# Optimization experiments

Hardware: AMD Instinct MI355X
Metric: run time of the kernel (lower is better)

The kernel has to match this reference:

```python
import jax, jax.numpy as jnp
import numpy as np

NUM_TREES = 150
ARITY = 4
DEPTH = 4
NUM_LEVELS = DEPTH + 1  # leaves (level 0) ... root (level DEPTH)
VOCAB = 10000
SUBTOK = 8
EMB_DIM = 256
HID = 256
NUM_CLASSES = 2


def _build_forest():
    # perfect ARITY-ary tree, level-order indexing; edges point child -> parent
    n = (ARITY ** (DEPTH + 1) - 1) // (ARITY - 1)  # 341
    src = np.arange(1, n)
    dst = (src - 1) // ARITY
    depth_of = np.zeros(n, dtype=np.int64)
    for j in range(1, n):
        depth_of[j] = depth_of[(j - 1) // ARITY] + 1
    level_of = DEPTH - depth_of  # leaves = 0, processed first (topo order)
    offs = np.arange(NUM_TREES) * n
    edge_src = (src[None, :] + offs[:, None]).ravel().astype(np.int32)
    edge_dst = (dst[None, :] + offs[:, None]).ravel().astype(np.int32)
    node_level = np.tile(level_of, NUM_TREES).astype(np.int32)
    graph_id = np.repeat(np.arange(NUM_TREES), n).astype(np.int32)
    leaf_mask = (node_level == 0).astype(np.int32)
    return edge_src, edge_dst, node_level, graph_id, leaf_mask, NUM_TREES * n


def setup_inputs() -> dict:
    key = jax.random.key(0)
    ks = jax.random.split(key, 16)
    es, ed, lvl, gid, lm, N = _build_forest()
    s_e = 1.0 / np.sqrt(EMB_DIM)
    s_h = 1.0 / np.sqrt(HID)
    s_f = 1.0 / np.sqrt(2 * HID)
    return {
        "node_feat1": jax.random.randint(ks[0], (N, SUBTOK), 0, VOCAB, dtype=jnp.int32),
        "node_feat2": jax.random.randint(ks[1], (N, SUBTOK), 0, VOCAB, dtype=jnp.int32),
        "emb1": jax.random.normal(ks[2], (VOCAB, EMB_DIM), jnp.float32) * 0.02,
        "emb2": jax.random.normal(ks[3], (VOCAB, EMB_DIM), jnp.float32) * 0.02,
        "W_iou1": jax.random.normal(ks[4], (EMB_DIM, 3 * HID), jnp.float32) * s_e,
        "W_iou2": jax.random.normal(ks[5], (EMB_DIM, 3 * HID), jnp.float32) * s_e,
        "U_iou1": jax.random.normal(ks[6], (HID, 3 * HID), jnp.float32) * s_h,
        "U_iou2": jax.random.normal(ks[7], (HID, 3 * HID), jnp.float32) * s_h,
        "Uf_W1": jax.random.normal(ks[8], (HID, HID), jnp.float32) * s_h,
        "Uf_b1": jnp.zeros((HID,), jnp.float32),
        "Uf_W2": jax.random.normal(ks[9], (HID, HID), jnp.float32) * s_h,
        "Uf_b2": jnp.zeros((HID,), jnp.float32),
        "b_iou1": jnp.zeros((3 * HID,), jnp.float32),
        "b_iou2": jnp.zeros((3 * HID,), jnp.float32),
        "Wf": jax.random.normal(ks[10], (2 * HID, NUM_CLASSES), jnp.float32) * s_f,
        "bf": jnp.zeros((NUM_CLASSES,), jnp.float32),
        "edge_src": jnp.asarray(es),
        "edge_dst": jnp.asarray(ed),
        "node_level": jnp.asarray(lvl),
        "graph_id": jnp.asarray(gid),
        "leaf_mask": jnp.asarray(lm),
    }


def _tree_lstm(iou0, U_iou, Uf_W, Uf_b, b_iou, edge_src, edge_dst, node_level):
    # ChildSum TreeLSTM, propagated level-by-level (leaves -> root)
    N = iou0.shape[0]
    h = jnp.zeros((N, HID), iou0.dtype)
    c = jnp.zeros((N, HID), iou0.dtype)
    for lvl in range(NUM_LEVELS):
        emask = (node_level[edge_dst] == lvl).astype(h.dtype)[:, None]  # [E,1]
        hs = h[edge_src] * emask  # children h (already computed at lower levels)
        f = jax.nn.sigmoid(hs @ Uf_W + Uf_b)  # per-edge forget gate
        h_tild = jax.ops.segment_sum(hs, edge_dst, num_segments=N)
        c_sum = jax.ops.segment_sum(f * c[edge_src] * emask, edge_dst, num_segments=N)
        has_child = jax.ops.segment_sum(emask, edge_dst, num_segments=N) > 0  # [N,1]
        # DGL semantics: reduce overwrites iou for internal nodes; leaves keep W_iou(x)*mask
        iou = jnp.where(has_child, h_tild @ U_iou, iou0) + b_iou
        i, o, u = jnp.split(iou, 3, axis=1)
        c_new = jax.nn.sigmoid(i) * jnp.tanh(u) + c_sum
        h_new = jax.nn.sigmoid(o) * jnp.tanh(c_new)
        at = (node_level == lvl)[:, None]
        h = jnp.where(at, h_new, h)
        c = jnp.where(at, c_new, c)
    return h


def _branch(node_feat, emb, W_iou, U_iou, Uf_W, Uf_b, b_iou,
            leaf_mask, edge_src, edge_dst, node_level, graph_id):
    embeds = emb[node_feat].mean(axis=1)  # subtoken mean pooling -> [N, EMB_DIM]
    iou0 = (embeds @ W_iou) * leaf_mask.astype(embeds.dtype)[:, None]
    h = _tree_lstm(iou0, U_iou, Uf_W, Uf_b, b_iou, edge_src, edge_dst, node_level)
    s = jax.ops.segment_sum(h, graph_id, num_segments=NUM_TREES)
    cnt = jax.ops.segment_sum(jnp.ones((h.shape[0],), h.dtype), graph_id, num_segments=NUM_TREES)
    return jax.nn.relu(s / cnt[:, None])  # mean graph readout + relu


def reference(node_feat1, node_feat2, emb1, emb2, W_iou1, W_iou2, U_iou1, U_iou2,
              Uf_W1, Uf_b1, Uf_W2, Uf_b2, b_iou1, b_iou2, Wf, bf,
              edge_src, edge_dst, node_level, graph_id, leaf_mask):
    m1 = _branch(node_feat1, emb1, W_iou1, U_iou1, Uf_W1, Uf_b1, b_iou1,
                 leaf_mask, edge_src, edge_dst, node_level, graph_id)
    m2 = _branch(node_feat2, emb2, W_iou2, U_iou2, Uf_W2, Uf_b2, b_iou2,
                 leaf_mask, edge_src, edge_dst, node_level, graph_id)
    logits = jax.nn.leaky_relu(jnp.concatenate([m1, m2], axis=1) @ Wf + bf, 0.01)
    return jax.nn.softmax(logits, axis=-1)
```

## Files before the change

### kernel.cpp

```cpp
#include <hip/hip_runtime.h>

#define NT 150
#define NPT 341
#define LEAF0 85
#define NL (NT*256)
#define NN (NT*NPT)
#define VOCAB 10000

typedef __attribute__((ext_vector_type(8))) short short8;
typedef __attribute__((ext_vector_type(4))) float floatx4;

__device__ __forceinline__ float sigf(float x){ return 1.0f/(1.0f+__expf(-x)); }
__device__ __forceinline__ float bf2f(ushort u){ union{unsigned i; float f;} v; v.i = ((unsigned)u)<<16; return v.f; }
__device__ __forceinline__ ushort f2bf(float x){ union{float f; unsigned i;} v; v.f = x; return (ushort)((v.i + 0x7fff + ((v.i>>16)&1))>>16); }

__global__ __launch_bounds__(256) void convW_k(
    const float* __restrict__ W1, const float* __restrict__ U1, const float* __restrict__ F1,
    const float* __restrict__ W2, const float* __restrict__ U2, const float* __restrict__ F2,
    ushort* Wt1, ushort* Ut1, ushort* Ft1, ushort* Wt2, ushort* Ut2, ushort* Ft2){
  __shared__ float T[32][33];
  const float* src; ushort* dst; int N;
  switch (blockIdx.z){
    case 0: src=W1; dst=Wt1; N=768; break;
    case 1: src=U1; dst=Ut1; N=768; break;
    case 2: src=F1; dst=Ft1; N=256; break;
    case 3: src=W2; dst=Wt2; N=768; break;
    case 4: src=U2; dst=Ut2; N=768; break;
    default: src=F2; dst=Ft2; N=256; break;
  }
  int n0 = blockIdx.x*32; if (n0 >= N) return;
  int k0 = blockIdx.y*32;
  int nl = threadIdx.x & 31, kb = threadIdx.x >> 5;
  #pragma unroll
  for (int i=0;i<4;i++){ int kk = kb*4+i; T[kk][nl] = src[(size_t)(k0+kk)*N + n0 + nl]; }
  __syncthreads();
  #pragma unroll
  for (int i=0;i<4;i++){ int nn = kb*4+i; dst[(size_t)(n0+nn)*256 + k0 + nl] = f2bf(T[nl][nn]); }
}

__global__ __launch_bounds__(256) void convE_k(
    const float* __restrict__ e1, const float* __restrict__ e2,
    ushort* __restrict__ E1, ushort* __restrict__ E2){
  const float* s = blockIdx.y ? e2 : e1;
  ushort* d = blockIdx.y ? E2 : E1;
  size_t i = ((size_t)blockIdx.x*256 + threadIdx.x)*4;
  float4 v = *(const float4*)&s[i];
  d[i+0]=f2bf(v.x); d[i+1]=f2bf(v.y); d[i+2]=f2bf(v.z); d[i+3]=f2bf(v.w);
}

__global__ __launch_bounds__(256) void embed_k(
    const int* __restrict__ f1, const int* __restrict__ f2,
    const ushort* __restrict__ E1, const ushort* __restrict__ E2,
    ushort* __restrict__ h1, ushort* __restrict__ h2){
  int br = blockIdx.y;
  const int* feat = br ? f2 : f1;
  const ushort* E = br ? E2 : E1;
  ushort* h = br ? h2 : h1;
  int t = threadIdx.x;
  int leaf = blockIdx.x*16 + (t>>4);
  int seg = t & 15;
  int tree = leaf >> 8;
  size_t node = (size_t)tree*NPT + LEAF0 + (leaf & 255);
  const int* f = feat + node*8;
  float s[16];
  #pragma unroll
  for (int q=0;q<16;q++) s[q]=0.f;
  #pragma unroll
  for (int j=0;j<8;j++){
    const ushort* row = E + (size_t)f[j]*256 + seg*16;
    short8 a = *(const short8*)row;
    short8 b = *(const short8*)(row+8);
    #pragma unroll
    for (int q=0;q<8;q++){ s[q]+=bf2f((ushort)a[q]); s[8+q]+=bf2f((ushort)b[q]); }
  }
  short8 o1, o2;
  #pragma unroll
  for (int q=0;q<8;q++){ o1[q]=(short)f2bf(s[q]*0.125f); o2[q]=(short)f2bf(s[8+q]*0.125f); }
  ushort* dst = h + node*256 + seg*16;
  *(short8*)dst = o1; *(short8*)(dst+8) = o2;
}

__global__ __launch_bounds__(1024) void leaf_gemm(
    const ushort* __restrict__ Wt1, const float* __restrict__ b1,
    const ushort* __restrict__ Wt2, const float* __restrict__ b2,
    ushort* __restrict__ h1, ushort* __restrict__ c1,
    ushort* __restrict__ h2, ushort* __restrict__ c2){
  __shared__ __attribute__((aligned(16))) ushort As[8][64*40];
  int br = blockIdx.y;
  const ushort* Wt = br ? Wt2 : Wt1;
  const float* biou = br ? b2 : b1;
  ushort* h = br ? h2 : h1;
  ushort* c = br ? c2 : c1;
  int tid = threadIdx.x;
  int lane = tid & 63, wav = tid >> 6, quad = lane >> 4, l15 = lane & 15;
  int rowbase = blockIdx.x*64;

  {
    int row = tid >> 4, seg = tid & 15;
    int leaf = rowbase + row;
    int tree = leaf >> 8;
    size_t node = (size_t)tree*NPT + LEAF0 + (leaf & 255);
    const ushort* src = h + node*256 + seg*16;
    short8 a = *(const short8*)src;
    short8 b = *(const short8*)(src+8);
    int cch = seg >> 1, off = (seg & 1)*16;
    *(short8*)&As[cch][row*40 + off]     = a;
    *(short8*)&As[cch][row*40 + off + 8] = b;
  }
  __syncthreads();

  floatx4 acc[3][4];
  #pragma unroll
  for (int g=0;g<3;g++)
    #pragma unroll
    for (int r=0;r<4;r++) acc[g][r] = (floatx4){0.f,0.f,0.f,0.f};

  const ushort* bp0 = Wt + (size_t)(0*256 + wav*16 + l15)*256 + quad*8;
  const ushort* bp1 = Wt + (size_t)(1*256 + wav*16 + l15)*256 + quad*8;
  const ushort* bp2 = Wt + (size_t)(2*256 + wav*16 + l15)*256 + quad*8;

  #pragma unroll
  for (int cch=0; cch<8; cch++){
    short8 b0 = *(const short8*)(bp0 + cch*32);
    short8 b1 = *(const short8*)(bp1 + cch*32);
    short8 b2 = *(const short8*)(bp2 + cch*32);
    #pragma unroll
    for (int r=0;r<4;r++){
      short8 a = *(const short8*)&As[cch][(16*r + l15)*40 + quad*8];
      acc[0][r] = __builtin_amdgcn_mfma_f32_16x16x32_bf16(a, b0, acc[0][r], 0,0,0);
      acc[1][r] = __builtin_amdgcn_mfma_f32_16x16x32_bf16(a, b1, acc[1][r], 0,0,0);
      acc[2][r] = __builtin_amdgcn_mfma_f32_16x16x32_bf16(a, b2, acc[2][r], 0,0,0);
    }
  }
  int hc = wav*16 + l15;
  float bi = biou[hc], bo = biou[256+hc], bu = biou[512+hc];
  #pragma unroll
  for (int r=0;r<4;r++){
    #pragma unroll
    for (int reg=0;reg<4;reg++){
      int leaf = rowbase + 16*r + quad*4 + reg;
      int tree = leaf >> 8;
      size_t node = (size_t)tree*NPT + LEAF0 + (leaf & 255);
      float iv = acc[0][r][reg] + bi;
      float ov = acc[1][r][reg] + bo;
      float uv = acc[2][r][reg] + bu;
      float cc = sigf(iv)*tanhf(uv);
      float hh = sigf(ov)*tanhf(cc);
      h[node*256 + hc] = f2bf(hh);
      c[node*256 + hc] = f2bf(cc);
    }
  }
}

__global__ __launch_bounds__(256) void level_k(
    const ushort* __restrict__ Ut1, const ushort* __restrict__ Ft1,
    const float* __restrict__ Ufb1, const float* __restrict__ bi1,
    const ushort* __restrict__ Ut2, const ushort* __restrict__ Ft2,
    const float* __restrict__ Ufb2, const float* __restrict__ bi2,
    ushort* __restrict__ h1, ushort* __restrict__ c1,
    ushort* __restrict__ h2, ushort* __restrict__ c2,
    int M, int shift, int base){
  __shared__ __attribute__((aligned(16))) ushort Ch[8][64*40];
  int br = blockIdx.z;
  const ushort* Ut = br ? Ut2 : Ut1;
  const ushort* Ft = br ? Ft2 : Ft1;
  const float* Ufb = br ? Ufb2 : Ufb1;
  const float* biou = br ? bi2 : bi1;
  ushort* h = br ? h2 : h1;
  ushort* c = br ? c2 : c1;
  int tid = threadIdx.x;
  int lane = tid & 63, wav = tid >> 6, quad = lane >> 4, l15 = lane & 15;
  int m0 = blockIdx.x*16, cb = blockIdx.y;
  int mask = (1<<shift)-1;

  {
    int cl = tid >> 2, q4 = tid & 3;
    int sm = m0 + (cl >> 2); if (sm > M-1) sm = M-1;
    int stree = sm >> shift, sloc = base + (sm & mask);
    const ushort* sgp = h + ((size_t)stree*NPT + 4*sloc + 1 + (cl & 3))*256 + q4*8;
    #pragma unroll
    for (int cc=0;cc<8;cc++)
      *(short8*)&Ch[cc][cl*40 + q4*8] = *(const short8*)(sgp + cc*32);
  }
  __syncthreads();

  int col = cb*64 + wav*16 + l15;
  const ushort* bfp = Ft + (size_t)col*256 + quad*8;
  const ushort* bp0 = Ut + (size_t)(0*256 + col)*256 + quad*8;
  const ushort* bp1 = Ut + (size_t)(256 + col)*256 + quad*8;
  const ushort* bp2 = Ut + (size_t)(512 + col)*256 + quad*8;

  floatx4 af[4], ai[4], ao[4], au[4];
  #pragma unroll
  for (int r=0;r<4;r++){
    af[r] = (floatx4){0.f,0.f,0.f,0.f}; ai[r] = (floatx4){0.f,0.f,0.f,0.f};
    ao[r] = (floatx4){0.f,0.f,0.f,0.f}; au[r] = (floatx4){0.f,0.f,0.f,0.f};
  }

  #pragma unroll
  for (int cc=0; cc<8; cc++){
    short8 Bf = *(const short8*)(bfp + cc*32);
    short8 Bi = *(const short8*)(bp0 + cc*32);
    short8 Bo = *(const short8*)(bp1 + cc*32);
    short8 Bu = *(const short8*)(bp2 + cc*32);
    #pragma unroll
    for (int r=0;r<4;r++){
      short8 a = *(const short8*)&Ch[cc][(16*r + l15)*40 + quad*8];
      af[r] = __builtin_amdgcn_mfma_f32_16x16x32_bf16(a, Bf, af[r], 0,0,0);
      ai[r] = __builtin_amdgcn_mfma_f32_16x16x32_bf16(a, Bi, ai[r], 0,0,0);
      ao[r] = __builtin_amdgcn_mfma_f32_16x16x32_bf16(a, Bo, ao[r], 0,0,0);
      au[r] = __builtin_amdgcn_mfma_f32_16x16x32_bf16(a, Bu, au[r], 0,0,0);
    }
  }

  float ufb = Ufb[col];
  float bI = biou[col], bO = biou[256+col], bU = biou[512+col];
  #pragma unroll
  for (int r=0;r<4;r++){
    int m = m0 + 4*r + quad;
    int mm = m < M ? m : M-1;
    int tree = mm >> shift, loc = base + (mm & mask);
    size_t ch0 = ((size_t)tree*NPT + 4*loc + 1)*256 + col;
    float cs = 0.f;
    #pragma unroll
    for (int reg=0;reg<4;reg++)
      cs += sigf(af[r][reg] + ufb) * bf2f(c[ch0 + (size_t)reg*256]);
    float iv = ai[r][0]+ai[r][1]+ai[r][2]+ai[r][3] + bI;
    float ov = ao[r][0]+ao[r][1]+ao[r][2]+ao[r][3] + bO;
    float uv = au[r][0]+au[r][1]+au[r][2]+au[r][3] + bU;
    float cn = sigf(iv)*tanhf(uv) + cs;
    float hn = sigf(ov)*tanhf(cn);
    if (m < M){
      size_t off = ((size_t)tree*NPT + loc)*256 + col;
      h[off] = f2bf(hn);
      c[off] = f2bf(cn);
    }
  }
}

__global__ __launch_bounds__(256) void readout_k(
    const ushort* __restrict__ h1, const ushort* __restrict__ h2,
    float* __restrict__ mp1, float* __restrict__ mp2){
  int br = blockIdx.z, part = blockIdx.y, tree = blockIdx.x;
  const ushort* h = br ? h2 : h1;
  float* mp = br ? mp2 : mp1;
  int t = threadIdx.x;
  int start = part*85;
  int cnt = (part==3) ? 86 : 85;
  const ushort* hp = h + ((size_t)tree*NPT + start)*256 + t;
  float s0=0.f,s1=0.f,s2=0.f,s3=0.f;
  int i = 0;
  for (; i+4<=cnt; i+=4){
    s0 += bf2f(hp[(size_t)(i+0)*256]); s1 += bf2f(hp[(size_t)(i+1)*256]);
    s2 += bf2f(hp[(size_t)(i+2)*256]); s3 += bf2f(hp[(size_t)(i+3)*256]);
  }
  for (; i<cnt; i++) s0 += bf2f(hp[(size_t)i*256]);
  mp[((size_t)tree*4 + part)*256 + t] = s0+s1+s2+s3;
}

__global__ __launch_bounds__(64) void final_k(const float* __restrict__ mp1,
    const float* __restrict__ mp2, const float* __restrict__ Wf,
    const float* __restrict__ bf, float* __restrict__ out){
  int tree = blockIdx.x; int t = threadIdx.x;
  float p0=0.f, p1=0.f;
  for (int k=t;k<512;k+=64){
    const float* mp = (k<256) ? mp1 : mp2;
    int kk = k & 255;
    size_t b0 = ((size_t)tree*4)*256 + kk;
    float s = mp[b0] + mp[b0+256] + mp[b0+512] + mp[b0+768];
    float x = fmaxf(s*(1.0f/341.0f), 0.f);
    p0 += x*Wf[k*2+0]; p1 += x*Wf[k*2+1];
  }
  #pragma unroll
  for (int off=32; off>0; off>>=1){
    p0 += __shfl_down(p0, off);
    p1 += __shfl_down(p1, off);
  }
  if (t==0){
    float l0 = p0+bf[0], l1 = p1+bf[1];
    l0 = (l0>0.f)?l0:0.01f*l0;
    l1 = (l1>0.f)?l1:0.01f*l1;
    float mx = fmaxf(l0,l1);
    float e0 = __expf(l0-mx), e1 = __expf(l1-mx);
    float inv = 1.0f/(e0+e1);
    out[tree*2+0] = e0*inv; out[tree*2+1] = e1*inv;
  }
}

extern "C" void kernel_launch(void* const* d_in, const int* in_sizes, int n_in,
                              void* d_out, int out_size, void* d_ws, size_t ws_size,
                              hipStream_t stream) {
  const int*   feat1 = (const int*)  d_in[0];
  const int*   feat2 = (const int*)  d_in[1];
  const float* emb1  = (const float*)d_in[2];
  const float* emb2  = (const float*)d_in[3];
  const float* Wiou1 = (const float*)d_in[4];
  const float* Wiou2 = (const float*)d_in[5];
  const float* Uiou1 = (const float*)d_in[6];
  const float* Uiou2 = (const float*)d_in[7];
  const float* UfW1  = (const float*)d_in[8];
  const float* Ufb1  = (const float*)d_in[9];
  const float* UfW2  = (const float*)d_in[10];
  const float* Ufb2  = (const float*)d_in[11];
  const float* biou1 = (const float*)d_in[12];
  const float* biou2 = (const float*)d_in[13];
  const float* Wf    = (const float*)d_in[14];
  const float* bfv   = (const float*)d_in[15];
  float* out = (float*)d_out;

  char* ws = (char*)d_ws;
  ushort* h1  = (ushort*)ws;  ws += (size_t)NN*256*2;
  ushort* h2  = (ushort*)ws;  ws += (size_t)NN*256*2;
  ushort* c1  = (ushort*)ws;  ws += (size_t)NN*256*2;
  ushort* c2  = (ushort*)ws;  ws += (size_t)NN*256*2;
  ushort* E1  = (ushort*)ws;  ws += (size_t)VOCAB*256*2;
  ushort* E2  = (ushort*)ws;  ws += (size_t)VOCAB*256*2;
  ushort* Wt1 = (ushort*)ws;  ws += 768*256*2;
  ushort* Ut1 = (ushort*)ws;  ws += 768*256*2;
  ushort* Ft1 = (ushort*)ws;  ws += 256*256*2;
  ushort* Wt2 = (ushort*)ws;  ws += 768*256*2;
  ushort* Ut2 = (ushort*)ws;  ws += 768*256*2;
  ushort* Ft2 = (ushort*)ws;  ws += 256*256*2;
  float*  mp1 = (float*)ws;   ws += (size_t)NT*4*256*4;
  float*  mp2 = (float*)ws;   ws += (size_t)NT*4*256*4;

  convW_k<<<dim3(24, 8, 6), 256, 0, stream>>>(Wiou1, Uiou1, UfW1, Wiou2, Uiou2, UfW2,
                                              Wt1, Ut1, Ft1, Wt2, Ut2, Ft2);
  convE_k<<<dim3(2500, 2), 256, 0, stream>>>(emb1, emb2, E1, E2);
  embed_k<<<dim3(NL/16, 2), 256, 0, stream>>>(feat1, feat2, E1, E2, h1, h2);
  leaf_gemm<<<dim3(NL/64, 2), 1024, 0, stream>>>(Wt1, biou1, Wt2, biou2, h1, c1, h2, c2);

  const int lvlM[4]     = {9600, 2400, 600, 150};
  const int lvlShift[4] = {6, 4, 2, 0};
  const int lvlBase[4]  = {21, 5, 1, 0};
  for (int l=0;l<4;l++){
    int gx = (lvlM[l] + 15)/16;
    level_k<<<dim3(gx, 4, 2), 256, 0, stream>>>(Ut1, Ft1, Ufb1, biou1,
                                                Ut2, Ft2, Ufb2, biou2,
                                                h1, c1, h2, c2,
                                                lvlM[l], lvlShift[l], lvlBase[l]);
  }
  readout_k<<<dim3(NT, 4, 2), 256, 0, stream>>>(h1, h2, mp1, mp2);
  final_k<<<NT, 64, 0, stream>>>(mp1, mp2, Wf, bfv, out);
}
```

Measured before the change: 380.8 us.

## Fuse embedding pooling into leaf GEMM and reuse child tiles across column blocks

```diff
diff --git a/kernel.cpp b/kernel.cpp
--- a/kernel.cpp
+++ b/kernel.cpp
@@ -48,45 +48,17 @@
   d[i+0]=f2bf(v.x); d[i+1]=f2bf(v.y); d[i+2]=f2bf(v.z); d[i+3]=f2bf(v.w);
 }
 
-__global__ __launch_bounds__(256) void embed_k(
+__global__ __launch_bounds__(1024) void leaf_k(
     const int* __restrict__ f1, const int* __restrict__ f2,
     const ushort* __restrict__ E1, const ushort* __restrict__ E2,
-    ushort* __restrict__ h1, ushort* __restrict__ h2){
-  int br = blockIdx.y;
-  const int* feat = br ? f2 : f1;
-  const ushort* E = br ? E2 : E1;
-  ushort* h = br ? h2 : h1;
-  int t = threadIdx.x;
-  int leaf = blockIdx.x*16 + (t>>4);
-  int seg = t & 15;
-  int tree = leaf >> 8;
-  size_t node = (size_t)tree*NPT + LEAF0 + (leaf & 255);
-  const int* f = feat + node*8;
-  float s[16];
-  #pragma unroll
-  for (int q=0;q<16;q++) s[q]=0.f;
-  #pragma unroll
-  for (int j=0;j<8;j++){
-    const ushort* row = E + (size_t)f[j]*256 + seg*16;
-    short8 a = *(const short8*)row;
-    short8 b = *(const short8*)(row+8);
-    #pragma unroll
-    for (int q=0;q<8;q++){ s[q]+=bf2f((ushort)a[q]); s[8+q]+=bf2f((ushort)b[q]); }
-  }
-  short8 o1, o2;
-  #pragma unroll
-  for (int q=0;q<8;q++){ o1[q]=(short)f2bf(s[q]*0.125f); o2[q]=(short)f2bf(s[8+q]*0.125f); }
-  ushort* dst = h + node*256 + seg*16;
-  *(short8*)dst = o1; *(short8*)(dst+8) = o2;
-}
-
-__global__ __launch_bounds__(1024) void leaf_gemm(
     const ushort* __restrict__ Wt1, const float* __restrict__ b1,
     const ushort* __restrict__ Wt2, const float* __restrict__ b2,
     ushort* __restrict__ h1, ushort* __restrict__ c1,
     ushort* __restrict__ h2, ushort* __restrict__ c2){
   __shared__ __attribute__((aligned(16))) ushort As[8][64*40];
   int br = blockIdx.y;
+  const int* feat = br ? f2 : f1;
+  const ushort* E = br ? E2 : E1;
   const ushort* Wt = br ? Wt2 : Wt1;
   const float* biou = br ? b2 : b1;
   ushort* h = br ? h2 : h1;
@@ -100,12 +72,24 @@
     int leaf = rowbase + row;
     int tree = leaf >> 8;
     size_t node = (size_t)tree*NPT + LEAF0 + (leaf & 255);
-    const ushort* src = h + node*256 + seg*16;
-    short8 a = *(const short8*)src;
-    short8 b = *(const short8*)(src+8);
+    const int* f = feat + node*8;
+    float s[16];
+    #pragma unroll
+    for (int q=0;q<16;q++) s[q]=0.f;
+    #pragma unroll
+    for (int j=0;j<8;j++){
+      const ushort* rp = E + (size_t)f[j]*256 + seg*16;
+      short8 a = *(const short8*)rp;
+      short8 b = *(const short8*)(rp+8);
+      #pragma unroll
+      for (int q=0;q<8;q++){ s[q]+=bf2f((ushort)a[q]); s[8+q]+=bf2f((ushort)b[q]); }
+    }
+    short8 o1, o2;
+    #pragma unroll
+    for (int q=0;q<8;q++){ o1[q]=(short)f2bf(s[q]*0.125f); o2[q]=(short)f2bf(s[8+q]*0.125f); }
     int cch = seg >> 1, off = (seg & 1)*16;
-    *(short8*)&As[cch][row*40 + off]     = a;
-    *(short8*)&As[cch][row*40 + off + 8] = b;
+    *(short8*)&As[cch][row*40 + off]     = o1;
+    *(short8*)&As[cch][row*40 + off + 8] = o2;
   }
   __syncthreads();
 
@@ -159,7 +143,7 @@
     const float* __restrict__ Ufb2, const float* __restrict__ bi2,
     ushort* __restrict__ h1, ushort* __restrict__ c1,
     ushort* __restrict__ h2, ushort* __restrict__ c2,
-    int M, int shift, int base){
+    int M, int shift, int base, int ncb){
   __shared__ __attribute__((aligned(16))) ushort Ch[8][64*40];
   int br = blockIdx.z;
   const ushort* Ut = br ? Ut2 : Ut1;
@@ -170,7 +154,8 @@
   ushort* c = br ? c2 : c1;
   int tid = threadIdx.x;
   int lane = tid & 63, wav = tid >> 6, quad = lane >> 4, l15 = lane & 15;
-  int m0 = blockIdx.x*16, cb = blockIdx.y;
+  int m0 = blockIdx.x*16;
+  int cb0 = blockIdx.y*ncb;
   int mask = (1<<shift)-1;
 
   {
@@ -184,56 +169,58 @@
   }
   __syncthreads();
 
-  int col = cb*64 + wav*16 + l15;
-  const ushort* bfp = Ft + (size_t)col*256 + quad*8;
-  const ushort* bp0 = Ut + (size_t)(0*256 + col)*256 + quad*8;
-  const ushort* bp1 = Ut + (size_t)(256 + col)*256 + quad*8;
-  const ushort* bp2 = Ut + (size_t)(512 + col)*256 + quad*8;
-
-  floatx4 af[4], ai[4], ao[4], au[4];
-  #pragma unroll
-  for (int r=0;r<4;r++){
-    af[r] = (floatx4){0.f,0.f,0.f,0.f}; ai[r] = (floatx4){0.f,0.f,0.f,0.f};
-    ao[r] = (floatx4){0.f,0.f,0.f,0.f}; au[r] = (floatx4){0.f,0.f,0.f,0.f};
-  }
-
-  #pragma unroll
-  for (int cc=0; cc<8; cc++){
-    short8 Bf = *(const short8*)(bfp + cc*32);
-    short8 Bi = *(const short8*)(bp0 + cc*32);
-    short8 Bo = *(const short8*)(bp1 + cc*32);
-    short8 Bu = *(const short8*)(bp2 + cc*32);
+  for (int p=0; p<ncb; p++){
+    int col = (cb0+p)*64 + wav*16 + l15;
+    const ushort* bfp = Ft + (size_t)col*256 + quad*8;
+    const ushort* bp0 = Ut + (size_t)(0*256 + col)*256 + quad*8;
+    const ushort* bp1 = Ut + (size_t)(256 + col)*256 + quad*8;
+    const ushort* bp2 = Ut + (size_t)(512 + col)*256 + quad*8;
+
+    floatx4 af[4], ai[4], ao[4], au[4];
     #pragma unroll
     for (int r=0;r<4;r++){
-      short8 a = *(const short8*)&Ch[cc][(16*r + l15)*40 + quad*8];
-      af[r] = __builtin_amdgcn_mfma_f32_16x16x32_bf16(a, Bf, af[r], 0,0,0);
-      ai[r] = __builtin_amdgcn_mfma_f32_16x16x32_bf16(a, Bi, ai[r], 0,0,0);
-      ao[r] = __builtin_amdgcn_mfma_f32_16x16x32_bf16(a, Bo, ao[r], 0,0,0);
-      au[r] = __builtin_amdgcn_mfma_f32_16x16x32_bf16(a, Bu, au[r], 0,0,0);
-    }
-  }
-
-  float ufb = Ufb[col];
-  float bI = biou[col], bO = biou[256+col], bU = biou[512+col];
-  #pragma unroll
-  for (int r=0;r<4;r++){
-    int m = m0 + 4*r + quad;
-    int mm = m < M ? m : M-1;
-    int tree = mm >> shift, loc = base + (mm & mask);
-    size_t ch0 = ((size_t)tree*NPT + 4*loc + 1)*256 + col;
-    float cs = 0.f;
-    #pragma unroll
-    for (int reg=0;reg<4;reg++)
-      cs += sigf(af[r][reg] + ufb) * bf2f(c[ch0 + (size_t)reg*256]);
-    float iv = ai[r][0]+ai[r][1]+ai[r][2]+ai[r][3] + bI;
-    float ov = ao[r][0]+ao[r][1]+ao[r][2]+ao[r][3] + bO;
-    float uv = au[r][0]+au[r][1]+au[r][2]+au[r][3] + bU;
-    float cn = sigf(iv)*tanhf(uv) + cs;
-    float hn = sigf(ov)*tanhf(cn);
-    if (m < M){
-      size_t off = ((size_t)tree*NPT + loc)*256 + col;
-      h[off] = f2bf(hn);
-      c[off] = f2bf(cn);
+      af[r] = (floatx4){0.f,0.f,0.f,0.f}; ai[r] = (floatx4){0.f,0.f,0.f,0.f};
+      ao[r] = (floatx4){0.f,0.f,0.f,0.f}; au[r] = (floatx4){0.f,0.f,0.f,0.f};
+    }
+
+    #pragma unroll
+    for (int cc=0; cc<8; cc++){
+      short8 Bf = *(const short8*)(bfp + cc*32);
+      short8 Bi = *(const short8*)(bp0 + cc*32);
+      short8 Bo = *(const short8*)(bp1 + cc*32);
+      short8 Bu = *(const short8*)(bp2 + cc*32);
+      #pragma unroll
+      for (int r=0;r<4;r++){
+        short8 a = *(const short8*)&Ch[cc][(16*r + l15)*40 + quad*8];
+        af[r] = __builtin_amdgcn_mfma_f32_16x16x32_bf16(a, Bf, af[r], 0,0,0);
+        ai[r] = __builtin_amdgcn_mfma_f32_16x16x32_bf16(a, Bi, ai[r], 0,0,0);
+        ao[r] = __builtin_amdgcn_mfma_f32_16x16x32_bf16(a, Bo, ao[r], 0,0,0);
+        au[r] = __builtin_amdgcn_mfma_f32_16x16x32_bf16(a, Bu, au[r], 0,0,0);
+      }
+    }
+
+    float ufb = Ufb[col];
+    float bI = biou[col], bO = biou[256+col], bU = biou[512+col];
+    #pragma unroll
+    for (int r=0;r<4;r++){
+      int m = m0 + 4*r + quad;
+      int mm = m < M ? m : M-1;
+      int tree = mm >> shift, loc = base + (mm & mask);
+      size_t ch0 = ((size_t)tree*NPT + 4*loc + 1)*256 + col;
+      float cs = 0.f;
+      #pragma unroll
+      for (int reg=0;reg<4;reg++)
+        cs += sigf(af[r][reg] + ufb) * bf2f(c[ch0 + (size_t)reg*256]);
+      float iv = ai[r][0]+ai[r][1]+ai[r][2]+ai[r][3] + bI;
+      float ov = ao[r][0]+ao[r][1]+ao[r][2]+ao[r][3] + bO;
+      float uv = au[r][0]+au[r][1]+au[r][2]+au[r][3] + bU;
+      float cn = sigf(iv)*tanhf(uv) + cs;
+      float hn = sigf(ov)*tanhf(cn);
+      if (m < M){
+        size_t off = ((size_t)tree*NPT + loc)*256 + col;
+        h[off] = f2bf(hn);
+        c[off] = f2bf(cn);
+      }
     }
   }
 }
@@ -324,21 +311,23 @@
   float*  mp1 = (float*)ws;   ws += (size_t)NT*4*256*4;
   float*  mp2 = (float*)ws;   ws += (size_t)NT*4*256*4;
 
+  convE_k<<<dim3(2500, 2), 256, 0, stream>>>(emb1, emb2, E1, E2);
   convW_k<<<dim3(24, 8, 6), 256, 0, stream>>>(Wiou1, Uiou1, UfW1, Wiou2, Uiou2, UfW2,
                                               Wt1, Ut1, Ft1, Wt2, Ut2, Ft2);
-  convE_k<<<dim3(2500, 2), 256, 0, stream>>>(emb1, emb2, E1, E2);
-  embed_k<<<dim3(NL/16, 2), 256, 0, stream>>>(feat1, feat2, E1, E2, h1, h2);
-  leaf_gemm<<<dim3(NL/64, 2), 1024, 0, stream>>>(Wt1, biou1, Wt2, biou2, h1, c1, h2, c2);
+  leaf_k<<<dim3(NL/64, 2), 1024, 0, stream>>>(feat1, feat2, E1, E2,
+                                              Wt1, biou1, Wt2, biou2, h1, c1, h2, c2);
 
   const int lvlM[4]     = {9600, 2400, 600, 150};
   const int lvlShift[4] = {6, 4, 2, 0};
   const int lvlBase[4]  = {21, 5, 1, 0};
+  const int lvlGy[4]    = {1, 1, 2, 4};
+  const int lvlNcb[4]   = {4, 4, 2, 1};
   for (int l=0;l<4;l++){
     int gx = (lvlM[l] + 15)/16;
-    level_k<<<dim3(gx, 4, 2), 256, 0, stream>>>(Ut1, Ft1, Ufb1, biou1,
-                                                Ut2, Ft2, Ufb2, biou2,
-                                                h1, c1, h2, c2,
-                                                lvlM[l], lvlShift[l], lvlBase[l]);
+    level_k<<<dim3(gx, lvlGy[l], 2), 256, 0, stream>>>(Ut1, Ft1, Ufb1, biou1,
+                                                       Ut2, Ft2, Ufb2, biou2,
+                                                       h1, c1, h2, c2,
+                                                       lvlM[l], lvlShift[l], lvlBase[l], lvlNcb[l]);
   }
   readout_k<<<dim3(NT, 4, 2), 256, 0, stream>>>(h1, h2, mp1, mp2);
   final_k<<<NT, 64, 0, stream>>>(mp1, mp2, Wf, bfv, out);
```

Result: slower. 445.8 us (+17.1%).
